# Optimization experiments

Measured on AMD Instinct MI355X. Metric: run time of the kernel, lower is better.

Reference implementation:

```python
import jax, jax.numpy as jnp
import numpy as np
import math

DIM = 1024
NUM_HEADS = 16


def setup_inputs() -> dict:
    key = jax.random.key(0)
    ks = jax.random.split(key, 6)
    B, S, D = 2, 2048, DIM
    return {
        "q": jax.random.normal(ks[0], (B, S, D), dtype=jnp.float32),
        "k": jax.random.normal(ks[1], (B, S, D), dtype=jnp.float32),
        "v": jax.random.normal(ks[2], (B, S, D), dtype=jnp.float32),
        "wq": jax.random.normal(ks[3], (D, D), dtype=jnp.float32),
        "wk": jax.random.normal(ks[4], (D, D), dtype=jnp.float32),
        "wv": jax.random.normal(ks[5], (D, D), dtype=jnp.float32),
    }


def reference(q, k, v, wq, wk, wv):
    B, S, D = q.shape
    H = NUM_HEADS
    hd = D // H
    # projections: [B,S,D] @ [D,D]
    qp = (q @ wq).reshape(B, H, S, hd)  # NOTE: direct reshape, as in the original
    kp = (k @ wk).reshape(B, H, S, hd)
    vp = (v @ wv).reshape(B, H, S, hd)
    scale = 1.0 / math.sqrt(D)  # original scales by sqrt(dim), not sqrt(head_dim)
    att = jnp.einsum("bhqd,bhkd->bhqk", qp, kp) * scale  # [B,H,S,S]
    att = jax.nn.softmax(att, axis=-1)
    out = jnp.einsum("bhqk,bhkd->bhqd", att, vp)  # [B,H,S,hd]
    out = out.transpose(0, 2, 1, 3).reshape(B, S, D)
    return out
```

## Files before the change

### kernel.cpp

```cpp
#include <hip/hip_runtime.h>
#include <hip/hip_bf16.h>
#include <stdint.h>

#define DIMD 1024
#define SEQ  2048
#define NH   16
#define MROWS 4096

typedef __bf16 bf16_t;
typedef bf16_t bf16x8 __attribute__((ext_vector_type(8)));
typedef float  f32x4  __attribute__((ext_vector_type(4)));
typedef unsigned short u16;
typedef unsigned short u16x4 __attribute__((ext_vector_type(4)));
typedef unsigned short u16x8 __attribute__((ext_vector_type(8)));
typedef unsigned int   u32;
typedef u32 u32x2 __attribute__((ext_vector_type(2)));

static __device__ __forceinline__ f32x4 mfma16(bf16x8 a, bf16x8 b, f32x4 c) {
    return __builtin_amdgcn_mfma_f32_16x16x32_bf16(a, b, c, 0, 0, 0);
}

static __device__ __forceinline__ float fast_exp2(float x) {
#if __has_builtin(__builtin_amdgcn_exp2f)
    return __builtin_amdgcn_exp2f(x);
#else
    return exp2f(x);
#endif
}

#define GLD16(gsrc, ldst) __builtin_amdgcn_global_load_lds(                    \
    (const __attribute__((address_space(1))) unsigned int*)(gsrc),             \
    (__attribute__((address_space(3))) unsigned int*)(ldst), 16, 0, 0)

static __device__ __forceinline__ void split_bf16(float x, u16& h, u16& l) {
    u32 u = __float_as_uint(x);
    u16 hu = (u16)(u >> 16);
    float xh = __uint_as_float((u32)hu << 16);
    float lo = x - xh;
    h = hu;
    l = (u16)(__float_as_uint(lo) >> 16);
}

static __device__ __forceinline__ u32 pack_bf16(float a, float b) {
    return (__float_as_uint(a) >> 16) | (__float_as_uint(b) & 0xffff0000u);
}

__global__ __launch_bounds__(256) void transWs3(
    const float* __restrict__ w0, const float* __restrict__ w1, const float* __restrict__ w2,
    u16* __restrict__ WTsH, u16* __restrict__ WTsL) {
    const int z = blockIdx.z;
    const float* W = z == 0 ? w0 : z == 1 ? w1 : w2;
    __shared__ u16 Hs[4096], Ls[4096];
    const int tid = threadIdx.x;
    const int kt = blockIdx.x, nt = blockIdx.y;
    const int n0 = nt * 128, k0 = kt * 32;
    #pragma unroll
    for (int i = 0; i < 4; i++) {
        int f = i * 256 + tid;
        int kr = f >> 5, nc4 = (f & 31) * 4;
        f32x4 w = *(const f32x4*)&W[(size_t)(k0 + kr) * DIMD + n0 + nc4];
        int cc = kr >> 3, e = kr & 7;
        #pragma unroll
        for (int j = 0; j < 4; j++) {
            u16 hh, ll; split_bf16(w[j], hh, ll);
            Hs[cc * 1024 + (nc4 + j) * 8 + e] = hh;
            Ls[cc * 1024 + (nc4 + j) * 8 + e] = ll;
        }
    }
    __syncthreads();
    const size_t base = (size_t)z * (DIMD * DIMD) + (size_t)(nt * 32 + kt) * 4096;
    #pragma unroll
    for (int i = 0; i < 2; i++) {
        int idx = (i * 256 + tid) * 8;
        *(u16x8*)(WTsH + base + idx) = *(const u16x8*)&Hs[idx];
        *(u16x8*)(WTsL + base + idx) = *(const u16x8*)&Ls[idx];
    }
}

__global__ __launch_bounds__(256, 3) void proj4(
    const float* __restrict__ xq, const float* __restrict__ xk, const float* __restrict__ xv,
    const u16* __restrict__ WTsH, const u16* __restrict__ WTsL,
    u16* __restrict__ qh, u16* __restrict__ ql,
    u16* __restrict__ kh, u16* __restrict__ kl,
    u16* __restrict__ vh) {

    const int z = blockIdx.z;
    const float* X = z == 0 ? xq : z == 1 ? xk : xv;
    const u16* BH = WTsH + (size_t)z * (DIMD * DIMD);
    const u16* BL = WTsL + (size_t)z * (DIMD * DIMD);
    u16* outH = z == 0 ? qh : z == 1 ? kh : vh;
    u16* outL = z == 0 ? ql : kl;
    const float oscale = z == 0 ? 0.0450842200278f : 1.0f;

    __shared__ u16 lds[16384];
    u16* AsH = lds;
    u16* AsL = lds + 4096;
    u16* BsH = lds + 8192;
    u16* BsL = lds + 12288;

    const int tid  = threadIdx.x;
    const int lane = tid & 63, wave = tid >> 6;
    const int quad = lane >> 4, l16 = lane & 15;
    const int wy = wave >> 1, wx = wave & 1;
    const int m0 = blockIdx.y * 128;
    const int n0 = blockIdx.x * 128;
    const size_t Bregion0 = (size_t)(blockIdx.x * 32) * 4096;

    f32x4 acc[4][4];
    #pragma unroll
    for (int mt = 0; mt < 4; mt++)
        #pragma unroll
        for (int nt = 0; nt < 4; nt++) acc[mt][nt] = (f32x4)0.0f;

    for (int kt = 0; kt < 32; kt++) {
        const int k0 = kt * 32;
        {
            const size_t rb = Bregion0 + (size_t)kt * 4096;
            int c0 = tid, c1 = 256 + tid;
            GLD16(BH + rb + c0 * 8, &BsH[c0 * 8]);
            GLD16(BH + rb + c1 * 8, &BsH[c1 * 8]);
            GLD16(BL + rb + c0 * 8, &BsL[c0 * 8]);
            GLD16(BL + rb + c1 * 8, &BsL[c1 * 8]);
        }
        #pragma unroll
        for (int i = 0; i < 4; i++) {
            int f = i * 256 + tid;
            int r = f >> 3, c4 = (f & 7) * 4;
            f32x4 a = *(const f32x4*)&X[(size_t)(m0 + r) * DIMD + k0 + c4];
            int cc = c4 >> 3, e = c4 & 7;
            u16x4 h4, l4;
            #pragma unroll
            for (int j = 0; j < 4; j++) {
                u16 hh, ll; split_bf16(a[j], hh, ll);
                h4[j] = hh; l4[j] = ll;
            }
            *(u16x4*)&AsH[(cc * 128 + r) * 8 + e] = h4;
            *(u16x4*)&AsL[(cc * 128 + r) * 8 + e] = l4;
        }
        __syncthreads();

        bf16x8 aH[4], aL[4], bH[4], bL[4];
        #pragma unroll
        for (int mt = 0; mt < 4; mt++) {
            int r = wy * 64 + mt * 16 + l16;
            aH[mt] = *(const bf16x8*)&AsH[(quad * 128 + r) * 8];
            aL[mt] = *(const bf16x8*)&AsL[(quad * 128 + r) * 8];
        }
        #pragma unroll
        for (int nt = 0; nt < 4; nt++) {
            int r = wx * 64 + nt * 16 + l16;
            bH[nt] = *(const bf16x8*)&BsH[(quad * 128 + r) * 8];
            bL[nt] = *(const bf16x8*)&BsL[(quad * 128 + r) * 8];
        }
        #pragma unroll
        for (int mt = 0; mt < 4; mt++)
            #pragma unroll
            for (int nt = 0; nt < 4; nt++) {
                acc[mt][nt] = mfma16(aH[mt], bH[nt], acc[mt][nt]);
                acc[mt][nt] = mfma16(aH[mt], bL[nt], acc[mt][nt]);
                acc[mt][nt] = mfma16(aL[mt], bH[nt], acc[mt][nt]);
            }
        __syncthreads();
    }

    #pragma unroll
    for (int mt = 0; mt < 4; mt++)
        #pragma unroll
        for (int nt = 0; nt < 4; nt++)
            #pragma unroll
            for (int r = 0; r < 4; r++) {
                int row = m0 + wy * 64 + mt * 16 + quad * 4 + r;
                int col = n0 + wx * 64 + nt * 16 + l16;
                u16 hh, ll; split_bf16(acc[mt][nt][r] * oscale, hh, ll);
                outH[(size_t)row * DIMD + col] = hh;
                if (z != 2) outL[(size_t)row * DIMD + col] = ll;
            }
}

__global__ __launch_bounds__(256) void transposeV(
    const u16* __restrict__ vh, u16* __restrict__ vt) {
    __shared__ u16 Ls[64][72];
    const int tid = threadIdx.x;
    const int bh = blockIdx.y;
    const int s0 = blockIdx.x * 64;
    const size_t slab = (size_t)bh * (SEQ * 64);
    #pragma unroll
    for (int i = 0; i < 2; i++) {
        int f = i * 256 + tid;
        int r = f >> 3, c = (f & 7) * 8;
        *(u16x8*)&Ls[r][c] = *(const u16x8*)(vh + slab + (size_t)(s0 + r) * 64 + c);
    }
    __syncthreads();
    #pragma unroll
    for (int i = 0; i < 2; i++) {
        int f = i * 256 + tid;
        int d = f >> 3, j = (f & 7) * 8;
        u16x8 o;
        #pragma unroll
        for (int jj = 0; jj < 8; jj++) o[jj] = Ls[j + jj][d];
        *(u16x8*)(vt + slab + (size_t)d * SEQ + s0 + j) = o;
    }
}

__global__ __launch_bounds__(256, 2) void flash4(
    const u16* __restrict__ qh, const u16* __restrict__ ql,
    const u16* __restrict__ kh, const u16* __restrict__ kl,
    const u16* __restrict__ vt,
    float* __restrict__ out) {

    __shared__ u16 KH[2][64][72], KL[2][64][72], VTs[2][64][72];
    __shared__ u16 Ps[4][32][72];

    const int tid  = threadIdx.x;
    const int lane = tid & 63, wv = tid >> 6;
    const int quad = lane >> 4, l16 = lane & 15;
    const int bh = blockIdx.y, b = bh >> 4, h = bh & 15;
    const size_t slab = (size_t)bh * (SEQ * 64);
    const int q0 = blockIdx.x * 128 + wv * 32;

    bf16x8 qfH[2][2], qfL[2][2];
    #pragma unroll
    for (int mq = 0; mq < 2; mq++) {
        const size_t rb = slab + (size_t)(q0 + mq * 16 + l16) * 64;
        #pragma unroll
        for (int kk = 0; kk < 2; kk++) {
            qfH[mq][kk] = *(const bf16x8*)(qh + rb + kk * 32 + quad * 8);
            qfL[mq][kk] = *(const bf16x8*)(ql + rb + kk * 32 + quad * 8);
        }
    }

    f32x4 O[2][4];
    float M[2] = {-3.0e38f, -3.0e38f}, L[2] = {0.0f, 0.0f};
    #pragma unroll
    for (int mq = 0; mq < 2; mq++)
        #pragma unroll
        for (int nv = 0; nv < 4; nv++) O[mq][nv] = (f32x4)0.0f;

    const int f0 = tid, f1 = 256 + tid;
    const int r0 = f0 >> 3, c0 = (f0 & 7) * 8;
    const int r1 = f1 >> 3, c1 = (f1 & 7) * 8;
    u16x8 s0, s1, s2, s3, s4, s5;

    {
        const int j0 = 0;
        s0 = *(const u16x8*)(kh + slab + (size_t)(j0 + r0) * 64 + c0);
        s1 = *(const u16x8*)(kh + slab + (size_t)(j0 + r1) * 64 + c1);
        s2 = *(const u16x8*)(kl + slab + (size_t)(j0 + r0) * 64 + c0);
        s3 = *(const u16x8*)(kl + slab + (size_t)(j0 + r1) * 64 + c1);
        s4 = *(const u16x8*)(vt + slab + (size_t)r0 * SEQ + j0 + c0);
        s5 = *(const u16x8*)(vt + slab + (size_t)r1 * SEQ + j0 + c1);
    }
    *(u16x8*)&KH[0][r0][c0] = s0;  *(u16x8*)&KH[0][r1][c1] = s1;
    *(u16x8*)&KL[0][r0][c0] = s2;  *(u16x8*)&KL[0][r1][c1] = s3;
    *(u16x8*)&VTs[0][r0][c0] = s4; *(u16x8*)&VTs[0][r1][c1] = s5;
    __syncthreads();

    for (int t = 0; t < 32; t++) {
        const int cur = t & 1;
        if (t < 31) {
            const int j0 = (t + 1) * 64;
            s0 = *(const u16x8*)(kh + slab + (size_t)(j0 + r0) * 64 + c0);
            s1 = *(const u16x8*)(kh + slab + (size_t)(j0 + r1) * 64 + c1);
            s2 = *(const u16x8*)(kl + slab + (size_t)(j0 + r0) * 64 + c0);
            s3 = *(const u16x8*)(kl + slab + (size_t)(j0 + r1) * 64 + c1);
            s4 = *(const u16x8*)(vt + slab + (size_t)r0 * SEQ + j0 + c0);
            s5 = *(const u16x8*)(vt + slab + (size_t)r1 * SEQ + j0 + c1);
        }

        f32x4 St[2][4];
        #pragma unroll
        for (int mq = 0; mq < 2; mq++)
            #pragma unroll
            for (int nt = 0; nt < 4; nt++) St[mq][nt] = (f32x4)0.0f;
        #pragma unroll
        for (int nt = 0; nt < 4; nt++) {
            const int rB = nt * 16 + l16;
            #pragma unroll
            for (int kk = 0; kk < 2; kk++) {
                bf16x8 kHf = *(const bf16x8*)&KH[cur][rB][kk * 32 + quad * 8];
                bf16x8 kLf = *(const bf16x8*)&KL[cur][rB][kk * 32 + quad * 8];
                #pragma unroll
                for (int mq = 0; mq < 2; mq++) {
                    St[mq][nt] = mfma16(kHf, qfH[mq][kk], St[mq][nt]);
                    St[mq][nt] = mfma16(kLf, qfH[mq][kk], St[mq][nt]);
                    St[mq][nt] = mfma16(kHf, qfL[mq][kk], St[mq][nt]);
                }
            }
        }

        #pragma unroll
        for (int mq = 0; mq < 2; mq++) {
            float mx = St[mq][0][0];
            #pragma unroll
            for (int nt = 0; nt < 4; nt++)
                #pragma unroll
                for (int r = 0; r < 4; r++) mx = fmaxf(mx, St[mq][nt][r]);
            mx = fmaxf(mx, __shfl_xor(mx, 16));
            mx = fmaxf(mx, __shfl_xor(mx, 32));
            float Mn = fmaxf(M[mq], mx);
            float al = fast_exp2(M[mq] - Mn);
            M[mq] = Mn;
            float rs = 0.0f;
            #pragma unroll
            for (int nt = 0; nt < 4; nt++)
                #pragma unroll
                for (int r = 0; r < 4; r++) {
                    float p = fast_exp2(St[mq][nt][r] - Mn);
                    St[mq][nt][r] = p;
                    rs += p;
                }
            rs += __shfl_xor(rs, 16);
            rs += __shfl_xor(rs, 32);
            L[mq] = L[mq] * al + rs;
            #pragma unroll
            for (int nv = 0; nv < 4; nv++) O[mq][nv] *= al;
            #pragma unroll
            for (int nt = 0; nt < 4; nt++) {
                u32x2 d;
                d[0] = pack_bf16(St[mq][nt][0], St[mq][nt][1]);
                d[1] = pack_bf16(St[mq][nt][2], St[mq][nt][3]);
                *(u32x2*)&Ps[wv][mq * 16 + l16][nt * 16 + quad * 4] = d;
            }
        }

        #pragma unroll
        for (int kk = 0; kk < 2; kk++) {
            bf16x8 pB[2];
            #pragma unroll
            for (int mq = 0; mq < 2; mq++)
                pB[mq] = *(const bf16x8*)&Ps[wv][mq * 16 + l16][kk * 32 + quad * 8];
            #pragma unroll
            for (int nv = 0; nv < 4; nv++) {
                bf16x8 vF = *(const bf16x8*)&VTs[cur][nv * 16 + l16][kk * 32 + quad * 8];
                #pragma unroll
                for (int mq = 0; mq < 2; mq++)
                    O[mq][nv] = mfma16(vF, pB[mq], O[mq][nv]);
            }
        }

        if (t < 31) {
            const int nb = cur ^ 1;
            *(u16x8*)&KH[nb][r0][c0] = s0;  *(u16x8*)&KH[nb][r1][c1] = s1;
            *(u16x8*)&KL[nb][r0][c0] = s2;  *(u16x8*)&KL[nb][r1][c1] = s3;
            *(u16x8*)&VTs[nb][r0][c0] = s4; *(u16x8*)&VTs[nb][r1][c1] = s5;
        }
        __syncthreads();
    }

    #pragma unroll
    for (int mq = 0; mq < 2; mq++) {
        float inv = 1.0f / L[mq];
        int row = q0 + mq * 16 + l16;
        size_t obase = ((size_t)(b * SEQ + row)) * DIMD + h * 64;
        #pragma unroll
        for (int nv = 0; nv < 4; nv++) {
            f32x4 o = O[mq][nv] * inv;
            *(f32x4*)&out[obase + nv * 16 + quad * 4] = o;
        }
    }
}

extern "C" void kernel_launch(void* const* d_in, const int* in_sizes, int n_in,
                              void* d_out, int out_size, void* d_ws, size_t ws_size,
                              hipStream_t stream) {
    const float* q  = (const float*)d_in[0];
    const float* k  = (const float*)d_in[1];
    const float* v  = (const float*)d_in[2];
    const float* wq = (const float*)d_in[3];
    const float* wk = (const float*)d_in[4];
    const float* wv = (const float*)d_in[5];
    float* out = (float*)d_out;

    char* ws = (char*)d_ws;
    const size_t MB = 1 << 20;
    u16* WTsH = (u16*)(ws + 0);
    u16* WTsL = (u16*)(ws + 6 * MB);
    u16* vt   = (u16*)(ws + 0);
    u16* qh = (u16*)(ws + 12 * MB);
    u16* ql = (u16*)(ws + 20 * MB);
    u16* kh = (u16*)(ws + 28 * MB);
    u16* kl = (u16*)(ws + 36 * MB);
    u16* vh = (u16*)(ws + 44 * MB);

    transWs3<<<dim3(32, 8, 3), 256, 0, stream>>>(wq, wk, wv, WTsH, WTsL);

    proj4<<<dim3(8, 32, 3), 256, 0, stream>>>(
        q, k, v, WTsH, WTsL, qh, ql, kh, kl, vh);

    transposeV<<<dim3(SEQ / 64, 2 * NH), 256, 0, stream>>>(vh, vt);

    flash4<<<dim3(SEQ / 128, 2 * NH), 256, 0, stream>>>(
        qh, ql, kh, kl, vt, out);
}
```

Measured before the change: 269.5 us.

## Split attention over two key halves with a combine kernel

```diff
diff --git a/kernel.cpp b/kernel.cpp
--- a/kernel.cpp
+++ b/kernel.cpp
@@ -6,6 +6,7 @@
 #define SEQ  2048
 #define NH   16
 #define MROWS 4096
+#define NQ   65536
 
 typedef __bf16 bf16_t;
 typedef bf16_t bf16x8 __attribute__((ext_vector_type(8)));
@@ -43,6 +44,14 @@
 
 static __device__ __forceinline__ u32 pack_bf16(float a, float b) {
     return (__float_as_uint(a) >> 16) | (__float_as_uint(b) & 0xffff0000u);
+}
+static __device__ __forceinline__ u32 pack_bf16_rn(float a, float b) {
+    u32 ua = __float_as_uint(a) + 0x8000u;
+    u32 ub = __float_as_uint(b) + 0x8000u;
+    return (ua >> 16) | (ub & 0xffff0000u);
+}
+static __device__ __forceinline__ float bf_to_f(u16 v) {
+    return __uint_as_float((u32)v << 16);
 }
 
 __global__ __launch_bounds__(256) void transWs3(
@@ -77,7 +86,7 @@
     }
 }
 
-__global__ __launch_bounds__(256, 3) void proj4(
+__global__ __launch_bounds__(256, 3) void proj6(
     const float* __restrict__ xq, const float* __restrict__ xk, const float* __restrict__ xv,
     const u16* __restrict__ WTsH, const u16* __restrict__ WTsL,
     u16* __restrict__ qh, u16* __restrict__ ql,
@@ -102,9 +111,9 @@
     const int lane = tid & 63, wave = tid >> 6;
     const int quad = lane >> 4, l16 = lane & 15;
     const int wy = wave >> 1, wx = wave & 1;
-    const int m0 = blockIdx.y * 128;
-    const int n0 = blockIdx.x * 128;
-    const size_t Bregion0 = (size_t)(blockIdx.x * 32) * 4096;
+    const int m0 = blockIdx.x * 128;
+    const int n0 = blockIdx.y * 128;
+    const size_t Bregion0 = (size_t)(blockIdx.y * 32) * 4096;
 
     f32x4 acc[4][4];
     #pragma unroll
@@ -202,21 +211,22 @@
     }
 }
 
-__global__ __launch_bounds__(256, 2) void flash4(
+__global__ __launch_bounds__(256, 3) void flash6(
     const u16* __restrict__ qh, const u16* __restrict__ ql,
     const u16* __restrict__ kh, const u16* __restrict__ kl,
     const u16* __restrict__ vt,
-    float* __restrict__ out) {
-
-    __shared__ u16 KH[2][64][72], KL[2][64][72], VTs[2][64][72];
+    u16* __restrict__ Opart, float* __restrict__ Mpart, float* __restrict__ Lpart) {
+
+    __shared__ u16 KH[64][72], KL[64][72], VTs[64][72];
     __shared__ u16 Ps[4][32][72];
 
     const int tid  = threadIdx.x;
     const int lane = tid & 63, wv = tid >> 6;
     const int quad = lane >> 4, l16 = lane & 15;
-    const int bh = blockIdx.y, b = bh >> 4, h = bh & 15;
+    const int bh = blockIdx.x, z = blockIdx.z;
     const size_t slab = (size_t)bh * (SEQ * 64);
-    const int q0 = blockIdx.x * 128 + wv * 32;
+    const int q0 = blockIdx.y * 128 + wv * 32;
+    const int jbase = z * 1024;
 
     bf16x8 qfH[2][2], qfL[2][2];
     #pragma unroll
@@ -242,7 +252,7 @@
     u16x8 s0, s1, s2, s3, s4, s5;
 
     {
-        const int j0 = 0;
+        const int j0 = jbase;
         s0 = *(const u16x8*)(kh + slab + (size_t)(j0 + r0) * 64 + c0);
         s1 = *(const u16x8*)(kh + slab + (size_t)(j0 + r1) * 64 + c1);
         s2 = *(const u16x8*)(kl + slab + (size_t)(j0 + r0) * 64 + c0);
@@ -250,15 +260,14 @@
         s4 = *(const u16x8*)(vt + slab + (size_t)r0 * SEQ + j0 + c0);
         s5 = *(const u16x8*)(vt + slab + (size_t)r1 * SEQ + j0 + c1);
     }
-    *(u16x8*)&KH[0][r0][c0] = s0;  *(u16x8*)&KH[0][r1][c1] = s1;
-    *(u16x8*)&KL[0][r0][c0] = s2;  *(u16x8*)&KL[0][r1][c1] = s3;
-    *(u16x8*)&VTs[0][r0][c0] = s4; *(u16x8*)&VTs[0][r1][c1] = s5;
+    *(u16x8*)&KH[r0][c0] = s0;  *(u16x8*)&KH[r1][c1] = s1;
+    *(u16x8*)&KL[r0][c0] = s2;  *(u16x8*)&KL[r1][c1] = s3;
+    *(u16x8*)&VTs[r0][c0] = s4; *(u16x8*)&VTs[r1][c1] = s5;
     __syncthreads();
 
-    for (int t = 0; t < 32; t++) {
-        const int cur = t & 1;
-        if (t < 31) {
-            const int j0 = (t + 1) * 64;
+    for (int t = 0; t < 16; t++) {
+        if (t < 15) {
+            const int j0 = jbase + (t + 1) * 64;
             s0 = *(const u16x8*)(kh + slab + (size_t)(j0 + r0) * 64 + c0);
             s1 = *(const u16x8*)(kh + slab + (size_t)(j0 + r1) * 64 + c1);
             s2 = *(const u16x8*)(kl + slab + (size_t)(j0 + r0) * 64 + c0);
@@ -277,8 +286,8 @@
             const int rB = nt * 16 + l16;
             #pragma unroll
             for (int kk = 0; kk < 2; kk++) {
-                bf16x8 kHf = *(const bf16x8*)&KH[cur][rB][kk * 32 + quad * 8];
-                bf16x8 kLf = *(const bf16x8*)&KL[cur][rB][kk * 32 + quad * 8];
+                bf16x8 kHf = *(const bf16x8*)&KH[rB][kk * 32 + quad * 8];
+                bf16x8 kLf = *(const bf16x8*)&KL[rB][kk * 32 + quad * 8];
                 #pragma unroll
                 for (int mq = 0; mq < 2; mq++) {
                     St[mq][nt] = mfma16(kHf, qfH[mq][kk], St[mq][nt]);
@@ -297,9 +306,15 @@
                 for (int r = 0; r < 4; r++) mx = fmaxf(mx, St[mq][nt][r]);
             mx = fmaxf(mx, __shfl_xor(mx, 16));
             mx = fmaxf(mx, __shfl_xor(mx, 32));
-            float Mn = fmaxf(M[mq], mx);
-            float al = fast_exp2(M[mq] - Mn);
-            M[mq] = Mn;
+            float Mn = M[mq];
+            if (__any(mx > Mn)) {
+                Mn = fmaxf(Mn, mx);
+                float al = fast_exp2(M[mq] - Mn);
+                M[mq] = Mn;
+                L[mq] *= al;
+                #pragma unroll
+                for (int nv = 0; nv < 4; nv++) O[mq][nv] *= al;
+            }
             float rs = 0.0f;
             #pragma unroll
             for (int nt = 0; nt < 4; nt++)
@@ -311,9 +326,7 @@
                 }
             rs += __shfl_xor(rs, 16);
             rs += __shfl_xor(rs, 32);
-            L[mq] = L[mq] * al + rs;
-            #pragma unroll
-            for (int nv = 0; nv < 4; nv++) O[mq][nv] *= al;
+            L[mq] += rs;
             #pragma unroll
             for (int nt = 0; nt < 4; nt++) {
                 u32x2 d;
@@ -331,33 +344,59 @@
                 pB[mq] = *(const bf16x8*)&Ps[wv][mq * 16 + l16][kk * 32 + quad * 8];
             #pragma unroll
             for (int nv = 0; nv < 4; nv++) {
-                bf16x8 vF = *(const bf16x8*)&VTs[cur][nv * 16 + l16][kk * 32 + quad * 8];
+                bf16x8 vF = *(const bf16x8*)&VTs[nv * 16 + l16][kk * 32 + quad * 8];
                 #pragma unroll
                 for (int mq = 0; mq < 2; mq++)
                     O[mq][nv] = mfma16(vF, pB[mq], O[mq][nv]);
             }
         }
 
-        if (t < 31) {
-            const int nb = cur ^ 1;
-            *(u16x8*)&KH[nb][r0][c0] = s0;  *(u16x8*)&KH[nb][r1][c1] = s1;
-            *(u16x8*)&KL[nb][r0][c0] = s2;  *(u16x8*)&KL[nb][r1][c1] = s3;
-            *(u16x8*)&VTs[nb][r0][c0] = s4; *(u16x8*)&VTs[nb][r1][c1] = s5;
-        }
         __syncthreads();
-    }
-
+        if (t < 15) {
+            *(u16x8*)&KH[r0][c0] = s0;  *(u16x8*)&KH[r1][c1] = s1;
+            *(u16x8*)&KL[r0][c0] = s2;  *(u16x8*)&KL[r1][c1] = s3;
+            *(u16x8*)&VTs[r0][c0] = s4; *(u16x8*)&VTs[r1][c1] = s5;
+        }
+        __syncthreads();
+    }
+
+    const int qgb = bh * SEQ + q0;
     #pragma unroll
     for (int mq = 0; mq < 2; mq++) {
-        float inv = 1.0f / L[mq];
-        int row = q0 + mq * 16 + l16;
-        size_t obase = ((size_t)(b * SEQ + row)) * DIMD + h * 64;
+        const int qg = qgb + mq * 16 + l16;
         #pragma unroll
         for (int nv = 0; nv < 4; nv++) {
-            f32x4 o = O[mq][nv] * inv;
-            *(f32x4*)&out[obase + nv * 16 + quad * 4] = o;
-        }
-    }
+            u32x2 d;
+            d[0] = pack_bf16_rn(O[mq][nv][0], O[mq][nv][1]);
+            d[1] = pack_bf16_rn(O[mq][nv][2], O[mq][nv][3]);
+            *(u32x2*)(Opart + ((size_t)(z * NQ + qg)) * 64 + nv * 16 + quad * 4) = d;
+        }
+        if (quad == 0) {
+            Mpart[z * NQ + qg] = M[mq];
+            Lpart[z * NQ + qg] = L[mq];
+        }
+    }
+}
+
+__global__ __launch_bounds__(256) void combineK(
+    const u16* __restrict__ Opart, const float* __restrict__ Mpart,
+    const float* __restrict__ Lpart, float* __restrict__ out) {
+    int idx = blockIdx.x * 256 + threadIdx.x;
+    int qg = idx >> 4, c4 = (idx & 15) * 4;
+    float M0 = Mpart[qg], M1 = Mpart[NQ + qg];
+    float L0 = Lpart[qg], L1 = Lpart[NQ + qg];
+    float Ms = fmaxf(M0, M1);
+    float w0 = fast_exp2(M0 - Ms), w1 = fast_exp2(M1 - Ms);
+    float inv = 1.0f / (w0 * L0 + w1 * L1);
+    u16x4 a = *(const u16x4*)&Opart[(size_t)qg * 64 + c4];
+    u16x4 b = *(const u16x4*)&Opart[((size_t)NQ + qg) * 64 + c4];
+    f32x4 o;
+    #pragma unroll
+    for (int j = 0; j < 4; j++)
+        o[j] = (w0 * bf_to_f(a[j]) + w1 * bf_to_f(b[j])) * inv;
+    int bh = qg >> 11, s = qg & 2047;
+    int bb = bh >> 4, h = bh & 15;
+    *(f32x4*)&out[((size_t)(bb * SEQ + s)) * DIMD + h * 64 + c4] = o;
 }
 
 extern "C" void kernel_launch(void* const* d_in, const int* in_sizes, int n_in,
@@ -373,22 +412,27 @@
 
     char* ws = (char*)d_ws;
     const size_t MB = 1 << 20;
-    u16* WTsH = (u16*)(ws + 0);
-    u16* WTsL = (u16*)(ws + 6 * MB);
-    u16* vt   = (u16*)(ws + 0);
-    u16* qh = (u16*)(ws + 12 * MB);
-    u16* ql = (u16*)(ws + 20 * MB);
-    u16* kh = (u16*)(ws + 28 * MB);
-    u16* kl = (u16*)(ws + 36 * MB);
-    u16* vh = (u16*)(ws + 44 * MB);
+    u16* qh   = (u16*)(ws + 0 * MB);
+    u16* ql   = (u16*)(ws + 8 * MB);
+    u16* kh   = (u16*)(ws + 16 * MB);
+    u16* kl   = (u16*)(ws + 24 * MB);
+    u16* vh   = (u16*)(ws + 32 * MB);
+    u16* vt   = (u16*)(ws + 40 * MB);
+    u16* WTsH = (u16*)(ws + 48 * MB);
+    u16* WTsL = (u16*)(ws + 54 * MB);
+    u16*   Opart = (u16*)(ws + 48 * MB);
+    float* Mpart = (float*)(ws + 64 * MB);
+    float* Lpart = (float*)(ws + 64 * MB + 512 * 1024);
 
     transWs3<<<dim3(32, 8, 3), 256, 0, stream>>>(wq, wk, wv, WTsH, WTsL);
 
-    proj4<<<dim3(8, 32, 3), 256, 0, stream>>>(
+    proj6<<<dim3(32, 8, 3), 256, 0, stream>>>(
         q, k, v, WTsH, WTsL, qh, ql, kh, kl, vh);
 
     transposeV<<<dim3(SEQ / 64, 2 * NH), 256, 0, stream>>>(vh, vt);
 
-    flash4<<<dim3(SEQ / 128, 2 * NH), 256, 0, stream>>>(
-        qh, ql, kh, kl, vt, out);
-}
+    flash6<<<dim3(2 * NH, SEQ / 128, 2), 256, 0, stream>>>(
+        qh, ql, kh, kl, vt, Opart, Mpart, Lpart);
+
+    combineK<<<dim3(NQ * 16 / 256), 256, 0, stream>>>(Opart, Mpart, Lpart, out);
+}
```

Result: no change. 267.3 us (-0.8%).
